# Optimization experiments

Hardware: AMD Instinct MI355X
Metric: run time of the kernel (lower is better)

## Reference

```python
import jax, jax.numpy as jnp
import numpy as np

NUM_HEADS = 4
HEAD_DIM = 16  # out_channels // num_heads = 64 // 4
IN_C = 64
OUT_C = 64


def setup_inputs() -> dict:
    key = jax.random.key(0)
    k1, k2, k3 = jax.random.split(key, 3)
    x = jax.random.normal(k1, (2, IN_C, 64, 64), dtype=jnp.float32)
    # nn.Linear(in_channels, 3*out_channels): weight (3*OUT_C, IN_C), bias (3*OUT_C,)
    s = 1.0 / np.sqrt(IN_C)
    qkv_w = jax.random.uniform(k2, (3 * OUT_C, IN_C), minval=-s, maxval=s, dtype=jnp.float32)
    qkv_b = jax.random.uniform(k3, (3 * OUT_C,), minval=-s, maxval=s, dtype=jnp.float32)
    return {"x": x, "qkv_w": qkv_w, "qkv_b": qkv_b}


def reference(x, qkv_w, qkv_b):
    B, C, H, W = x.shape
    N = H * W
    # (B,C,H,W) -> (B,N,C)
    tokens = x.reshape(B, C, N).transpose(0, 2, 1)
    qkv = tokens @ qkv_w.T + qkv_b  # (B,N,3*OUT_C)
    q, k, v = jnp.split(qkv, 3, axis=-1)
    def to_heads(t):
        return t.reshape(B, N, NUM_HEADS, HEAD_DIM).transpose(0, 2, 1, 3)  # (B,h,N,d)
    q, k, v = to_heads(q), to_heads(k), to_heads(v)
    scale = 1.0 / np.sqrt(HEAD_DIM)
    attn = jnp.einsum('bhnd,bhmd->bhnm', q, k) * scale  # (B,h,N,N)
    attn = jax.nn.softmax(attn, axis=-1)
    # dropout is identity in eval mode
    out = jnp.einsum('bhnm,bhmd->bhnd', attn, v)  # (B,h,N,d)
    out = out.transpose(0, 2, 1, 3).reshape(B, N, OUT_C)  # (B,N,outC)
    out = out.transpose(0, 2, 1).reshape(B, OUT_C, H, W)
    return out
```

## Files before the change

kernel.cpp:

```cpp
#include <hip/hip_runtime.h>
#include <hip/hip_bf16.h>


#define NTOK 4096
#define HD   16
#define BH   8
#define QUART 1024
#define PITERS (QUART/32)

typedef __attribute__((ext_vector_type(4))) short short4v;
typedef __attribute__((ext_vector_type(8))) short short8v;
typedef __attribute__((ext_vector_type(4))) float float4v;
typedef __attribute__((ext_vector_type(4))) ushort ushort4v;
typedef __attribute__((ext_vector_type(2))) unsigned uint2v;

__device__ __forceinline__ ushort f2bf(float f) {
  unsigned u = __builtin_bit_cast(unsigned, f);
  u += 0x7fffu + ((u >> 16) & 1u);
  return (ushort)(u >> 16);
}

__device__ __forceinline__ float fast_exp2(float x) {
#if __has_builtin(__builtin_amdgcn_exp2f)
  return __builtin_amdgcn_exp2f(x);
#else
  return exp2f(x);
#endif
}

__device__ __forceinline__ short4v pack4_bf16(float a, float b, float c, float d) {
  __hip_bfloat162 lo = __float22bfloat162_rn(make_float2(a, b));
  __hip_bfloat162 hi = __float22bfloat162_rn(make_float2(c, d));
  unsigned ulo, uhi;
  __builtin_memcpy(&ulo, &lo, 4);
  __builtin_memcpy(&uhi, &hi, 4);
  uint2v u = { ulo, uhi };
  return __builtin_bit_cast(short4v, u);
}

#define QB_OFF 0
#define KB_OFF ((size_t)BH*NTOK*HD)
#define VT_OFF (2*(size_t)BH*NTOK*HD)

__global__ __launch_bounds__(192) void qkv_proj(
    const float* __restrict__ x, const float* __restrict__ w,
    const float* __restrict__ bias, ushort* __restrict__ wsu) {
  const int TOK = 8, TILES = 2;
  int blk = blockIdx.x;
  int b   = blk >> 8;
  int n00 = (blk & 255) * (TOK*TILES);
  int o   = threadIdx.x;

  float wr[64];
  const float4* w4 = reinterpret_cast<const float4*>(w + o*64);
  #pragma unroll
  for (int i = 0; i < 16; ++i) {
    float4 tt = w4[i];
    wr[4*i+0]=tt.x; wr[4*i+1]=tt.y; wr[4*i+2]=tt.z; wr[4*i+3]=tt.w;
  }
  float bb = bias[o];

  int part = o >> 6;
  int oo   = o & 63;
  int h    = oo >> 4;
  int dd   = oo & 15;
  int bh   = b*4 + h;
  const float QSCALE = 0.25f * 1.44269504f;

  ushort* Qt = wsu + QB_OFF;
  ushort* Kp = wsu + KB_OFF;
  ushort* Vp = wsu + VT_OFF;

  __shared__ float4 xs4[64][2];
  const float4* x4 = reinterpret_cast<const float4*>(x);

  #pragma unroll 1
  for (int tile = 0; tile < TILES; ++tile) {
    int n0 = n00 + tile*TOK;
    for (int idx = threadIdx.x; idx < 128; idx += 192) {
      int c = idx >> 1, t4 = idx & 1;
      xs4[c][t4] = x4[((size_t)b*64 + c)*(NTOK/4) + (n0 >> 2) + t4];
    }
    __syncthreads();

    #pragma unroll
    for (int t4 = 0; t4 < 2; ++t4) {
      float a[4] = {bb, bb, bb, bb};
      #pragma unroll
      for (int c = 0; c < 64; ++c) {
        float4 xv = xs4[c][t4];
        float wv = wr[c];
        a[0] = fmaf(xv.x, wv, a[0]);
        a[1] = fmaf(xv.y, wv, a[1]);
        a[2] = fmaf(xv.z, wv, a[2]);
        a[3] = fmaf(xv.w, wv, a[3]);
      }
      if (part == 0) {
        ushort4v vv = { f2bf(a[0]*QSCALE), f2bf(a[1]*QSCALE),
                        f2bf(a[2]*QSCALE), f2bf(a[3]*QSCALE) };
        *(ushort4v*)(Qt + ((size_t)bh*HD + dd)*NTOK + n0 + t4*4) = vv;
      } else if (part == 1) {
        #pragma unroll
        for (int j = 0; j < 4; ++j) {
          int n = n0 + t4*4 + j;
          size_t idx = (size_t)bh*NTOK*HD + (n >> 5)*512
                     + ((dd >> 2)*16 + (n & 15))*8 + ((n >> 4) & 1)*4 + (dd & 3);
          Kp[idx] = f2bf(a[j]);
        }
      } else {
        int m = n0 + t4*4;
        size_t idx = (size_t)bh*NTOK*HD + (m >> 5)*512
                   + (((m & 15) >> 2)*16 + dd)*8 + ((m >> 4) & 1)*4;
        ushort4v vv = { f2bf(a[0]), f2bf(a[1]), f2bf(a[2]), f2bf(a[3]) };
        *(ushort4v*)(Vp + idx) = vv;
      }
    }
    __syncthreads();
  }
}

__global__ __launch_bounds__(256, 4) void attn_mfma(
    const ushort* __restrict__ wsu, float* __restrict__ out) {
  const ushort* Qt = wsu + QB_OFF;
  const ushort* Kp = wsu + KB_OFF;
  const ushort* Vp = wsu + VT_OFF;

  int bh    = blockIdx.x >> 7;
  int qblk  = blockIdx.x & 127;
  int tid   = threadIdx.x;
  int quart = tid >> 6;
  int lane  = tid & 63;
  int lr    = lane & 15;
  int g4    = (lane >> 4) << 2;
  int qbase = qblk*32;

  __shared__ float comb[3][64][11];

  const ushort* Qh = Qt + (size_t)bh*HD*NTOK;
  const ushort* KhF = Kp + (size_t)bh*NTOK*HD + (size_t)quart*QUART*HD;
  const ushort* VhF = Vp + (size_t)bh*NTOK*HD + (size_t)quart*QUART*HD;

  short4v qf0, qf1;
  #pragma unroll
  for (int j = 0; j < 4; ++j) {
    qf0[j] = (short)Qh[(size_t)(g4+j)*NTOK + qbase      + lr];
    qf1[j] = (short)Qh[(size_t)(g4+j)*NTOK + qbase + 16 + lr];
  }

  const ushort* kp16 = KhF + lane*8;
  const ushort* vp16 = VhF + lane*8;

  float4v a0e = {0.f,0.f,0.f,0.f}, a0o = {0.f,0.f,0.f,0.f};
  float4v a1e = {0.f,0.f,0.f,0.f}, a1o = {0.f,0.f,0.f,0.f};
  float l0 = 0.f, l1 = 0.f;

#define ITER(kpr, vpr)                                                      \
  do {                                                                      \
    short4v ke = __builtin_shufflevector(kpr, kpr, 0,1,2,3);                \
    short4v ko = __builtin_shufflevector(kpr, kpr, 4,5,6,7);                \
    short4v ve = __builtin_shufflevector(vpr, vpr, 0,1,2,3);                \
    short4v vo = __builtin_shufflevector(vpr, vpr, 4,5,6,7);                \
    float4v zero = {0.f,0.f,0.f,0.f};                                       \
    __builtin_amdgcn_s_setprio(1);                                          \
    float4v s0e = __builtin_amdgcn_mfma_f32_16x16x16bf16_1k(ke, qf0, zero, 0,0,0); \
    float4v s0o = __builtin_amdgcn_mfma_f32_16x16x16bf16_1k(ko, qf0, zero, 0,0,0); \
    float4v s1e = __builtin_amdgcn_mfma_f32_16x16x16bf16_1k(ke, qf1, zero, 0,0,0); \
    float4v s1o = __builtin_amdgcn_mfma_f32_16x16x16bf16_1k(ko, qf1, zero, 0,0,0); \
    float p0e0 = fast_exp2(s0e[0]), p0e1 = fast_exp2(s0e[1]);               \
    float p0e2 = fast_exp2(s0e[2]), p0e3 = fast_exp2(s0e[3]);               \
    float p0o0 = fast_exp2(s0o[0]), p0o1 = fast_exp2(s0o[1]);               \
    float p0o2 = fast_exp2(s0o[2]), p0o3 = fast_exp2(s0o[3]);               \
    float p1e0 = fast_exp2(s1e[0]), p1e1 = fast_exp2(s1e[1]);               \
    float p1e2 = fast_exp2(s1e[2]), p1e3 = fast_exp2(s1e[3]);               \
    float p1o0 = fast_exp2(s1o[0]), p1o1 = fast_exp2(s1o[1]);               \
    float p1o2 = fast_exp2(s1o[2]), p1o3 = fast_exp2(s1o[3]);               \
    l0 += (p0e0 + p0e1) + (p0e2 + p0e3) + (p0o0 + p0o1) + (p0o2 + p0o3);    \
    l1 += (p1e0 + p1e1) + (p1e2 + p1e3) + (p1o0 + p1o1) + (p1o2 + p1o3);    \
    short4v pb0e = pack4_bf16(p0e0, p0e1, p0e2, p0e3);                      \
    short4v pb0o = pack4_bf16(p0o0, p0o1, p0o2, p0o3);                      \
    short4v pb1e = pack4_bf16(p1e0, p1e1, p1e2, p1e3);                      \
    short4v pb1o = pack4_bf16(p1o0, p1o1, p1o2, p1o3);                      \
    a0e = __builtin_amdgcn_mfma_f32_16x16x16bf16_1k(ve, pb0e, a0e, 0,0,0);  \
    a0o = __builtin_amdgcn_mfma_f32_16x16x16bf16_1k(vo, pb0o, a0o, 0,0,0);  \
    a1e = __builtin_amdgcn_mfma_f32_16x16x16bf16_1k(ve, pb1e, a1e, 0,0,0);  \
    a1o = __builtin_amdgcn_mfma_f32_16x16x16bf16_1k(vo, pb1o, a1o, 0,0,0);  \
    __builtin_amdgcn_s_setprio(0);                                          \
  } while (0)

  short8v kA = *(const short8v*)(kp16);
  short8v vA = *(const short8v*)(vp16);
  short8v kB = *(const short8v*)(kp16 + 512);
  short8v vB = *(const short8v*)(vp16 + 512);

  #pragma unroll 4
  for (int it2 = 0; it2 < PITERS/2; ++it2) {
    int oA = (2*it2 + 2) * 512;
    int oB = (2*it2 + 3) * 512;
    short8v nkA = *(const short8v*)(kp16 + oA);
    short8v nvA = *(const short8v*)(vp16 + oA);
    short8v nkB = *(const short8v*)(kp16 + oB);
    short8v nvB = *(const short8v*)(vp16 + oB);

    ITER(kA, vA);
    ITER(kB, vB);

    kA = nkA; vA = nvA; kB = nkB; vB = nvB;
  }
#undef ITER

  float o0[4], o1[4];
  #pragma unroll
  for (int r = 0; r < 4; ++r) {
    o0[r] = a0e[r] + a0o[r];
    o1[r] = a1e[r] + a1o[r];
  }

  if (quart != 0) {
    float* cp = &comb[quart-1][lane][0];
    cp[0] = o0[0]; cp[1] = o0[1]; cp[2] = o0[2]; cp[3] = o0[3];
    cp[4] = o1[0]; cp[5] = o1[1]; cp[6] = o1[2]; cp[7] = o1[3];
    cp[8] = l0;    cp[9] = l1;
  }
  __syncthreads();
  if (quart == 0) {
    #pragma unroll
    for (int wv = 0; wv < 3; ++wv) {
      const float* cp = &comb[wv][lane][0];
      o0[0] += cp[0]; o0[1] += cp[1]; o0[2] += cp[2]; o0[3] += cp[3];
      o1[0] += cp[4]; o1[1] += cp[5]; o1[2] += cp[6]; o1[3] += cp[7];
      l0 += cp[8];    l1 += cp[9];
    }
    l0 += __shfl_xor(l0, 16); l0 += __shfl_xor(l0, 32);
    l1 += __shfl_xor(l1, 16); l1 += __shfl_xor(l1, 32);
    float inv0 = 1.0f / l0, inv1 = 1.0f / l1;

    int b = bh >> 2, h = bh & 3;
    float* ob = out + ((size_t)(b*64 + h*16 + g4)) * NTOK;
    #pragma unroll
    for (int r = 0; r < 4; ++r) {
      ob[(size_t)r*NTOK + qbase      + lr] = o0[r] * inv0;
      ob[(size_t)r*NTOK + qbase + 16 + lr] = o1[r] * inv1;
    }
  }
}

extern "C" void kernel_launch(void* const* d_in, const int* in_sizes, int n_in,
                              void* d_out, int out_size, void* d_ws, size_t ws_size,
                              hipStream_t stream) {
  const float* x    = (const float*)d_in[0];
  const float* w    = (const float*)d_in[1];
  const float* bias = (const float*)d_in[2];
  float* out  = (float*)d_out;
  ushort* wsu = (ushort*)d_ws;

  qkv_proj <<<512,  192, 0, stream>>>(x, w, bias, wsu);
  attn_mfma<<<1024, 256, 0, stream>>>(wsu, out);
}
```

Measured before the change: 41.31 us.

## Restructure QKV projection: one thread per token, weights in LDS, more blocks

Rewrites the QKV projection so each block handles one (part, head) group of 16 output channels for 64 tokens. Each thread reads x directly from global memory with coalesced per-channel loads and computes 4 output channels, with the weights staged in LDS. The grid grows from 512 blocks to 1536 to expose more parallelism and drop the per-tile LDS staging of x. In exchange, x is re-read 12 times (once per output group) and the Q/V stores become scalar, strided writes.

```diff
diff --git a/kernel.cpp b/kernel.cpp
--- a/kernel.cpp
+++ b/kernel.cpp
@@ -42,80 +42,78 @@
 #define KB_OFF ((size_t)BH*NTOK*HD)
 #define VT_OFF (2*(size_t)BH*NTOK*HD)
 
-__global__ __launch_bounds__(192) void qkv_proj(
+__global__ __launch_bounds__(256) void qkv_proj(
     const float* __restrict__ x, const float* __restrict__ w,
     const float* __restrict__ bias, ushort* __restrict__ wsu) {
-  const int TOK = 8, TILES = 2;
-  int blk = blockIdx.x;
-  int b   = blk >> 8;
-  int n00 = (blk & 255) * (TOK*TILES);
-  int o   = threadIdx.x;
-
-  float wr[64];
-  const float4* w4 = reinterpret_cast<const float4*>(w + o*64);
-  #pragma unroll
-  for (int i = 0; i < 16; ++i) {
-    float4 tt = w4[i];
-    wr[4*i+0]=tt.x; wr[4*i+1]=tt.y; wr[4*i+2]=tt.z; wr[4*i+3]=tt.w;
-  }
-  float bb = bias[o];
-
-  int part = o >> 6;
-  int oo   = o & 63;
-  int h    = oo >> 4;
-  int dd   = oo & 15;
+  int tg   = blockIdx.x & 127;
+  int gg   = blockIdx.x >> 7;
+  int part = gg >> 2;
+  int h    = gg & 3;
+  int lane = threadIdx.x & 63;
+  int dg   = threadIdx.x >> 6;
+  int t    = tg*64 + lane;
+  int b    = t >> 12;
+  int np   = t & 4095;
   int bh   = b*4 + h;
   const float QSCALE = 0.25f * 1.44269504f;
 
-  ushort* Qt = wsu + QB_OFF;
-  ushort* Kp = wsu + KB_OFF;
-  ushort* Vp = wsu + VT_OFF;
-
-  __shared__ float4 xs4[64][2];
-  const float4* x4 = reinterpret_cast<const float4*>(x);
-
-  #pragma unroll 1
-  for (int tile = 0; tile < TILES; ++tile) {
-    int n0 = n00 + tile*TOK;
-    for (int idx = threadIdx.x; idx < 128; idx += 192) {
-      int c = idx >> 1, t4 = idx & 1;
-      xs4[c][t4] = x4[((size_t)b*64 + c)*(NTOK/4) + (n0 >> 2) + t4];
+  __shared__ float4 wls[16][16];
+  __shared__ float  bls[16];
+
+  {
+    const float4* wg = reinterpret_cast<const float4*>(w + (size_t)gg*16*64);
+    wls[threadIdx.x >> 4][threadIdx.x & 15] = wg[threadIdx.x];
+    if (threadIdx.x < 16) bls[threadIdx.x] = bias[gg*16 + threadIdx.x];
+  }
+  __syncthreads();
+
+  float acc0 = bls[dg*4+0], acc1 = bls[dg*4+1];
+  float acc2 = bls[dg*4+2], acc3 = bls[dg*4+3];
+  const float* xp = x + ((size_t)b*64)*NTOK + np;
+
+  #pragma unroll
+  for (int cc = 0; cc < 4; ++cc) {
+    float xr[16];
+    #pragma unroll
+    for (int i = 0; i < 16; ++i)
+      xr[i] = xp[(size_t)(cc*16 + i)*NTOK];
+    #pragma unroll
+    for (int i4 = 0; i4 < 4; ++i4) {
+      float4 w0 = wls[dg*4+0][cc*4+i4];
+      float4 w1 = wls[dg*4+1][cc*4+i4];
+      float4 w2 = wls[dg*4+2][cc*4+i4];
+      float4 w3 = wls[dg*4+3][cc*4+i4];
+      acc0 = fmaf(xr[i4*4+0], w0.x, acc0); acc0 = fmaf(xr[i4*4+1], w0.y, acc0);
+      acc0 = fmaf(xr[i4*4+2], w0.z, acc0); acc0 = fmaf(xr[i4*4+3], w0.w, acc0);
+      acc1 = fmaf(xr[i4*4+0], w1.x, acc1); acc1 = fmaf(xr[i4*4+1], w1.y, acc1);
+      acc1 = fmaf(xr[i4*4+2], w1.z, acc1); acc1 = fmaf(xr[i4*4+3], w1.w, acc1);
+      acc2 = fmaf(xr[i4*4+0], w2.x, acc2); acc2 = fmaf(xr[i4*4+1], w2.y, acc2);
+      acc2 = fmaf(xr[i4*4+2], w2.z, acc2); acc2 = fmaf(xr[i4*4+3], w2.w, acc2);
+      acc3 = fmaf(xr[i4*4+0], w3.x, acc3); acc3 = fmaf(xr[i4*4+1], w3.y, acc3);
+      acc3 = fmaf(xr[i4*4+2], w3.z, acc3); acc3 = fmaf(xr[i4*4+3], w3.w, acc3);
     }
-    __syncthreads();
-
-    #pragma unroll
-    for (int t4 = 0; t4 < 2; ++t4) {
-      float a[4] = {bb, bb, bb, bb};
-      #pragma unroll
-      for (int c = 0; c < 64; ++c) {
-        float4 xv = xs4[c][t4];
-        float wv = wr[c];
-        a[0] = fmaf(xv.x, wv, a[0]);
-        a[1] = fmaf(xv.y, wv, a[1]);
-        a[2] = fmaf(xv.z, wv, a[2]);
-        a[3] = fmaf(xv.w, wv, a[3]);
-      }
-      if (part == 0) {
-        ushort4v vv = { f2bf(a[0]*QSCALE), f2bf(a[1]*QSCALE),
-                        f2bf(a[2]*QSCALE), f2bf(a[3]*QSCALE) };
-        *(ushort4v*)(Qt + ((size_t)bh*HD + dd)*NTOK + n0 + t4*4) = vv;
-      } else if (part == 1) {
-        #pragma unroll
-        for (int j = 0; j < 4; ++j) {
-          int n = n0 + t4*4 + j;
-          size_t idx = (size_t)bh*NTOK*HD + (n >> 5)*512
-                     + ((dd >> 2)*16 + (n & 15))*8 + ((n >> 4) & 1)*4 + (dd & 3);
-          Kp[idx] = f2bf(a[j]);
-        }
-      } else {
-        int m = n0 + t4*4;
-        size_t idx = (size_t)bh*NTOK*HD + (m >> 5)*512
-                   + (((m & 15) >> 2)*16 + dd)*8 + ((m >> 4) & 1)*4;
-        ushort4v vv = { f2bf(a[0]), f2bf(a[1]), f2bf(a[2]), f2bf(a[3]) };
-        *(ushort4v*)(Vp + idx) = vv;
-      }
-    }
-    __syncthreads();
+  }
+
+  int dd0 = dg*4;
+  if (part == 0) {
+    ushort* Qt = wsu + QB_OFF + (size_t)bh*HD*NTOK + np;
+    Qt[(size_t)(dd0+0)*NTOK] = f2bf(acc0*QSCALE);
+    Qt[(size_t)(dd0+1)*NTOK] = f2bf(acc1*QSCALE);
+    Qt[(size_t)(dd0+2)*NTOK] = f2bf(acc2*QSCALE);
+    Qt[(size_t)(dd0+3)*NTOK] = f2bf(acc3*QSCALE);
+  } else if (part == 1) {
+    size_t idx = (size_t)bh*NTOK*HD + (size_t)(np >> 5)*512
+               + ((dd0 >> 2)*16 + (np & 15))*8 + ((np >> 4) & 1)*4;
+    ushort4v vv = { f2bf(acc0), f2bf(acc1), f2bf(acc2), f2bf(acc3) };
+    *(ushort4v*)(wsu + KB_OFF + idx) = vv;
+  } else {
+    size_t base = (size_t)bh*NTOK*HD + (size_t)(np >> 5)*512
+                + ((np >> 4) & 1)*4 + (np & 3);
+    ushort* Vp = wsu + VT_OFF + base;
+    Vp[(((np & 15) >> 2)*16 + dd0+0)*8] = f2bf(acc0);
+    Vp[(((np & 15) >> 2)*16 + dd0+1)*8] = f2bf(acc1);
+    Vp[(((np & 15) >> 2)*16 + dd0+2)*8] = f2bf(acc2);
+    Vp[(((np & 15) >> 2)*16 + dd0+3)*8] = f2bf(acc3);
   }
 }
 
@@ -253,6 +251,6 @@
   float* out  = (float*)d_out;
   ushort* wsu = (ushort*)d_ws;
 
-  qkv_proj <<<512,  192, 0, stream>>>(x, w, bias, wsu);
+  qkv_proj <<<1536, 256, 0, stream>>>(x, w, bias, wsu);
   attn_mfma<<<1024, 256, 0, stream>>>(wsu, out);
 }
```

Result: faster. 37.40 us (-9.5%).
